# Performance work log

Hardware: AMD Instinct MI355X
Metric: run time of the kernel (lower is better)

## Reference

```python
import jax, jax.numpy as jnp
import numpy as np

D_MODEL = 1024
NHEAD = 16
HEAD_DIM = D_MODEL // NHEAD  # 64
THETA = 10000.0


def apply_rope(t):
    # t: [B, H, S, D]. Interleaved-pair RoPE (lucidrains rotary-embedding-torch
    # rotate_queries_or_keys), positions = arange(S), theta = 10000.
    B, H, S, D = t.shape
    inv_freq = 1.0 / (THETA ** (jnp.arange(0, D, 2, dtype=jnp.float32) / D))  # [D/2]
    ang = jnp.arange(S, dtype=jnp.float32)[:, None] * inv_freq               # [S, D/2]
    cos = jnp.cos(ang).astype(t.dtype)
    sin = jnp.sin(ang).astype(t.dtype)
    tp = t.reshape(B, H, S, D // 2, 2)
    x1, x2 = tp[..., 0], tp[..., 1]
    rot = jnp.stack([x1 * cos - x2 * sin, x1 * sin + x2 * cos], axis=-1)
    return rot.reshape(B, H, S, D)


def setup_inputs() -> dict:
    key = jax.random.key(0)
    k0, k1, k2, k3, k4 = jax.random.split(key, 5)
    B, Sx, Sc = 2, 2048, 2048
    sc = 0.02  # weight init scale
    return {
        "x": jax.random.normal(k0, (B, Sx, D_MODEL), jnp.float32),
        "context": jax.random.normal(k1, (B, Sc, D_MODEL), jnp.float32),
        "Wq": jax.random.normal(k2, (D_MODEL, D_MODEL), jnp.float32) * sc,
        "Wv": jax.random.normal(k3, (D_MODEL, D_MODEL), jnp.float32) * sc,
        "Wo": jax.random.normal(k4, (D_MODEL, D_MODEL), jnp.float32) * sc,
        "bo": jnp.zeros((D_MODEL,), jnp.float32),
        "x_pos": jnp.arange(B * Sx, dtype=jnp.int64).reshape(B, Sx) % Sx,
        "context_pos": jnp.arange(B * Sc, dtype=jnp.int64).reshape(B, Sc) % Sc,
    }


def reference(x, context, Wq, Wv, Wo, bo, x_pos, context_pos):
    # x_pos/context_pos are unused when both streams use the internal
    # RotaryEmbedding (is_imu1=is_imu2=True), matching the original forward.
    B, Sx, _ = x.shape
    Sc = context.shape[1]
    q = (x @ Wq.T).reshape(B, Sx, NHEAD, HEAD_DIM).transpose(0, 2, 1, 3)
    # NOTE: original code uses projq (not projk) for keys — replicated here.
    k = (context @ Wq.T).reshape(B, Sc, NHEAD, HEAD_DIM).transpose(0, 2, 1, 3)
    v = (context @ Wv.T).reshape(B, Sc, NHEAD, HEAD_DIM).transpose(0, 2, 1, 3)
    q = apply_rope(q)
    k = apply_rope(k)
    scale = 1.0 / jnp.sqrt(jnp.asarray(HEAD_DIM, q.dtype))
    attn = jax.nn.softmax(jnp.einsum("bhqd,bhkd->bhqk", q, k) * scale, axis=-1)
    out = jnp.einsum("bhqk,bhkd->bhqd", attn, v)            # [B,H,Sx,hd]
    out = out.transpose(0, 2, 1, 3).reshape(B, Sx, D_MODEL)  # [B,Sx,d_model]
    return out @ Wo.T + bo
```

## Files before the change

kernel.cpp:

```cpp
#include <hip/hip_runtime.h>
#include <cmath>


typedef __bf16 bf16x8 __attribute__((ext_vector_type(8)));
typedef __bf16 bf16x4 __attribute__((ext_vector_type(4)));
typedef float f32x4 __attribute__((ext_vector_type(4)));
typedef float f32x16 __attribute__((ext_vector_type(16)));
typedef unsigned u32x4v __attribute__((ext_vector_type(4)));

#define MFMA(A, B, C) __builtin_amdgcn_mfma_f32_16x16x32_bf16(A, B, C, 0, 0, 0)
#define MFMA32(A, B, C) __builtin_amdgcn_mfma_f32_32x32x16_bf16(A, B, C, 0, 0, 0)
#define GLL16(g, l)                                                        \
  __builtin_amdgcn_global_load_lds(                                        \
      (const __attribute__((address_space(1))) unsigned int*)(g),          \
      (__attribute__((address_space(3))) unsigned int*)(l), 16, 0, 0)

#define WAITB(N)                                          \
  do {                                                    \
    asm volatile("s_waitcnt vmcnt(" #N ")" ::: "memory"); \
    __builtin_amdgcn_s_barrier();                         \
  } while (0)

__global__ __launch_bounds__(256) void cvt_all_kernel(
    const float* __restrict__ x, const float* __restrict__ ctx,
    const float* __restrict__ Wq, const float* __restrict__ Wv,
    const float* __restrict__ Wo, __bf16* __restrict__ xb, __bf16* __restrict__ cb,
    __bf16* __restrict__ Wqb, __bf16* __restrict__ Wvb, __bf16* __restrict__ Wob) {
  int base = blockIdx.x * 512 + threadIdx.x;
  const float* src;
  __bf16* dst;
  int off;
  if (base < 1048576) { src = x; dst = xb; off = 0; }
  else if (base < 2097152) { src = ctx; dst = cb; off = 1048576; }
  else if (base < 2359296) { src = Wq; dst = Wqb; off = 2097152; }
  else if (base < 2621440) { src = Wv; dst = Wvb; off = 2359296; }
  else { src = Wo; dst = Wob; off = 2621440; }
#pragma unroll
  for (int jj = 0; jj < 2; jj++) {
    int j = base - off + jj * 256;
    float4 f = ((const float4*)src)[j];
    bf16x4 o;
    o[0] = (__bf16)f.x; o[1] = (__bf16)f.y; o[2] = (__bf16)f.z; o[3] = (__bf16)f.w;
    ((bf16x4*)dst)[j] = o;
  }
}

__global__ __launch_bounds__(256) void gemm_proj(const __bf16* __restrict__ A0,
                                                 const __bf16* __restrict__ W0,
                                                 void* __restrict__ outQ,
                                                 void* __restrict__ outK,
                                                 void* __restrict__ outV) {
  const int tid = threadIdx.x;
  const int wave = tid >> 6, lane = tid & 63, quad = lane >> 4, l15 = lane & 15;
  const int mw = wave >> 1, nw = wave & 1;

  const int id = blockIdx.x;
  int m0, n0;
  const __bf16* A;
  const __bf16* W;
  bool vmode;
  if (id < 512) {
    const int xcd = id & 7, j = id >> 3;
    m0 = (xcd * 8 + (j & 7)) * 128;
    n0 = (j >> 3) * 128;
    A = A0;
    W = W0;
    vmode = false;
  } else {
    const int vid = id - 512;
    const int xcd = vid & 7, j = vid >> 3;
    m0 = (xcd * 4 + (j & 3)) * 128;
    n0 = (j >> 2) * 128;
    A = A0 + (size_t)4096 * 1024;
    W = W0 + (size_t)1024 * 1024;
    vmode = true;
  }

  __shared__ __attribute__((aligned(16))) __bf16 As[3][4096];
  __shared__ __attribute__((aligned(16))) __bf16 Ws[3][4096];

  int goff[2];
#pragma unroll
  for (int jj = 0; jj < 2; jj++) {
    const int s = jj * 256 + tid;
    const int row = s >> 2;
    const int kcg = (s & 3) ^ ((row >> 1) & 3);
    goff[jj] = row * 1024 + kcg * 8;
  }
  const __bf16* Ag = A + (size_t)m0 * 1024;
  const __bf16* Wg = W + (size_t)n0 * 1024;
  const int ldsoff0 = wave * 512;
  const int ldsoff1 = 2048 + wave * 512;

  const int sw = (l15 >> 1) & 3;
  int afoff[4], wfoff[4];
#pragma unroll
  for (int t = 0; t < 4; t++) {
    afoff[t] = (mw * 64 + t * 16 + l15) * 32 + (quad ^ sw) * 8;
    wfoff[t] = (nw * 64 + t * 16 + l15) * 32 + (quad ^ sw) * 8;
  }

  f32x4 acc[4][4] = {};

  auto stage = [&](int buf, int k0) {
    GLL16(Ag + goff[0] + k0, &As[buf][ldsoff0]);
    GLL16(Ag + goff[1] + k0, &As[buf][ldsoff1]);
    GLL16(Wg + goff[0] + k0, &Ws[buf][ldsoff0]);
    GLL16(Wg + goff[1] + k0, &Ws[buf][ldsoff1]);
  };
  auto compute = [&](int buf) {
    bf16x8 af[4], wf[4];
#pragma unroll
    for (int t = 0; t < 4; t++) af[t] = *(const bf16x8*)&As[buf][afoff[t]];
#pragma unroll
    for (int t = 0; t < 4; t++) wf[t] = *(const bf16x8*)&Ws[buf][wfoff[t]];
#pragma unroll
    for (int mt = 0; mt < 4; mt++)
#pragma unroll
      for (int nt = 0; nt < 4; nt++) acc[mt][nt] = MFMA(af[mt], wf[nt], acc[mt][nt]);
  };

  stage(0, 0);
  stage(1, 32);
  int buf = 0;
  for (int c = 0; c < 31; c++) {
    WAITB(4);
    if (c + 2 < 32) {
      int nb = buf + 2;
      if (nb >= 3) nb -= 3;
      stage(nb, (c + 2) * 32);
    }
    compute(buf);
    buf = (buf == 2) ? 0 : buf + 1;
  }
  WAITB(0);
  compute(buf);

  if (!vmode) {
    const int isK = (m0 >= 4096);
    __bf16* O = (__bf16*)(isK ? outK : outQ);
    const float qsc = isK ? 1.0f : 0.18033688f;
    const int mb = m0 & 4095;
#pragma unroll
    for (int nt = 0; nt < 4; nt++) {
      const int n = n0 + nw * 64 + nt * 16 + l15;
      const int h = n >> 6, d = n & 63, p = d >> 1;
      const float invf_rev =
          __builtin_amdgcn_exp2f(-((float)p * 0.41524101f + 2.6514961f));
#pragma unroll
      for (int mt = 0; mt < 4; mt++) {
#pragma unroll
        for (int r = 0; r < 4; r++) {
          const int row = mb + mw * 64 + mt * 16 + quad * 4 + r;
          const int s = row & 2047, b = row >> 11;
          float v = acc[mt][nt][r];
          float pv = __shfl_xor(v, 1, 64);
          float fr = __builtin_amdgcn_fractf((float)s * invf_rev);
          float sn = __builtin_amdgcn_sinf(fr);
          float cs = __builtin_amdgcn_cosf(fr);
          float res = (lane & 1) ? (pv * sn + v * cs) : (v * cs - pv * sn);
          O[((size_t)(b * 16 + h) * 2048 + s) * 64 + d] = (__bf16)(res * qsc);
        }
      }
    }
  } else {
    __bf16* O = (__bf16*)outV;
#pragma unroll
    for (int nt = 0; nt < 4; nt++) {
      const int n = n0 + nw * 64 + nt * 16 + l15;
      const int h = n >> 6, d = n & 63;
#pragma unroll
      for (int mt = 0; mt < 4; mt++) {
        const int rowb = m0 + mw * 64 + mt * 16 + quad * 4;
        const int s = rowb & 2047, b = rowb >> 11;
        bf16x4 o;
#pragma unroll
        for (int r = 0; r < 4; r++) o[r] = (__bf16)acc[mt][nt][r];
        *(bf16x4*)(O + ((size_t)(b * 16 + h) * 64 + d) * 2048 + s) = o;
      }
    }
  }
}

__global__ __launch_bounds__(256) void gemm_out(const __bf16* __restrict__ A,
                                                const __bf16* __restrict__ W,
                                                float* __restrict__ O,
                                                const float* __restrict__ bias) {
  const int tid = threadIdx.x;
  const int wave = tid >> 6, lane = tid & 63, quad = lane >> 4, l15 = lane & 15;
  const int mw = wave >> 1, nw = wave & 1;
  const int id = blockIdx.x;
  const int xcd = id & 7, j = id >> 3;
  const int m0 = (xcd * 4 + (j & 3)) * 128;
  const int n0 = (j >> 2) * 64;

  __shared__ __attribute__((aligned(16))) __bf16 As[3][4096];
  __shared__ __attribute__((aligned(16))) __bf16 Ws[3][2048];

  int goff[2];
#pragma unroll
  for (int jj = 0; jj < 2; jj++) {
    const int s = jj * 256 + tid;
    const int row = s >> 2;
    const int kcg = (s & 3) ^ ((row >> 1) & 3);
    goff[jj] = row * 1024 + kcg * 8;
  }
  const int wrow = tid >> 2;
  const int wkcg = (tid & 3) ^ ((wrow >> 1) & 3);
  const int goffw = wrow * 1024 + wkcg * 8;

  const __bf16* Ag = A + (size_t)m0 * 1024;
  const __bf16* Wg = W + (size_t)n0 * 1024;
  const int ldsoff0 = wave * 512;
  const int ldsoff1 = 2048 + wave * 512;

  const int sw = (l15 >> 1) & 3;
  int afoff[4], wfoff[2];
#pragma unroll
  for (int t = 0; t < 4; t++)
    afoff[t] = (mw * 64 + t * 16 + l15) * 32 + (quad ^ sw) * 8;
#pragma unroll
  for (int t = 0; t < 2; t++)
    wfoff[t] = (nw * 32 + t * 16 + l15) * 32 + (quad ^ sw) * 8;

  f32x4 acc[4][2] = {};

  auto stage = [&](int buf, int k0) {
    GLL16(Ag + goff[0] + k0, &As[buf][ldsoff0]);
    GLL16(Ag + goff[1] + k0, &As[buf][ldsoff1]);
    GLL16(Wg + goffw + k0, &Ws[buf][ldsoff0]);
  };
  auto compute = [&](int buf) {
    bf16x8 af[4], wf[2];
#pragma unroll
    for (int t = 0; t < 4; t++) af[t] = *(const bf16x8*)&As[buf][afoff[t]];
#pragma unroll
    for (int t = 0; t < 2; t++) wf[t] = *(const bf16x8*)&Ws[buf][wfoff[t]];
#pragma unroll
    for (int mt = 0; mt < 4; mt++)
#pragma unroll
      for (int nt = 0; nt < 2; nt++) acc[mt][nt] = MFMA(af[mt], wf[nt], acc[mt][nt]);
  };

  stage(0, 0);
  stage(1, 32);
  int buf = 0;
  for (int c = 0; c < 31; c++) {
    WAITB(3);
    if (c + 2 < 32) {
      int nb = buf + 2;
      if (nb >= 3) nb -= 3;
      stage(nb, (c + 2) * 32);
    }
    compute(buf);
    buf = (buf == 2) ? 0 : buf + 1;
  }
  WAITB(0);
  compute(buf);

#pragma unroll
  for (int nt = 0; nt < 2; nt++) {
    const int n = n0 + nw * 32 + nt * 16 + l15;
    const float bv = bias[n];
#pragma unroll
    for (int mt = 0; mt < 4; mt++) {
#pragma unroll
      for (int r = 0; r < 4; r++) {
        const int row = m0 + mw * 64 + mt * 16 + quad * 4 + r;
        O[(size_t)row * 1024 + n] = acc[mt][nt][r] + bv;
      }
    }
  }
}

__global__ __launch_bounds__(512, 4) void attn_kernel(const __bf16* __restrict__ Q,
                                                      const __bf16* __restrict__ K,
                                                      const __bf16* __restrict__ Vt,
                                                      __bf16* __restrict__ Aout) {
  const int tid = threadIdx.x;
  const int wave = tid >> 6, lane = tid & 63;
  const int l31 = lane & 31, hi = lane >> 5;
  const int qg = wave >> 1, kg = wave & 1;
  const int id = blockIdx.x;
  const int j = id >> 3;
  const int bh = ((id & 7) << 2) | (j & 3);
  const int q0 = (j >> 2) << 7;

  const __bf16* Qb = Q + (size_t)bh * (2048 * 64);
  const __bf16* Kb = K + (size_t)bh * (2048 * 64);
  const __bf16* Vb = Vt + (size_t)bh * (64 * 2048);

  __shared__ __attribute__((aligned(16))) __bf16 Kbuf[4][4096];
  __shared__ __attribute__((aligned(16))) __bf16 Vbuf[4][4096];

  bf16x8 qf[4];
  {
    const __bf16* qp = Qb + (size_t)(q0 + qg * 32 + l31) * 64 + hi * 8;
#pragma unroll
    for (int i = 0; i < 4; i++) qf[i] = *(const bf16x8*)(qp + i * 16);
  }

  const int s0 = wave * 64 + lane;
  const int r0 = s0 >> 3, c0 = (s0 & 7) ^ (r0 & 7);
  const __bf16* kgp = Kb + r0 * 64 + c0 * 8;
  const __bf16* vgp = Vb + r0 * 2048 + c0 * 8;
  const int klds = wave * 512;

  int koff[4];
  {
    const int rk = kg * 32 + l31;
#pragma unroll
    for (int i = 0; i < 4; i++) koff[i] = rk * 64 + (((2 * i + hi) ^ (rk & 7)) * 8);
  }
  int voff[2][2];
#pragma unroll
  for (int dt = 0; dt < 2; dt++) {
    const int rv = dt * 32 + l31;
#pragma unroll
    for (int ks = 0; ks < 2; ks++)
      voff[dt][ks] = rv * 64 + (((kg * 4 + ks * 2 + hi) ^ (rv & 7)) * 8);
  }

  f32x4 rs4 = {};
  f32x16 oacc[2] = {};

  auto stage = [&](int buf, int kt) {
    GLL16(kgp + kt * 64, &Kbuf[buf][klds]);
    GLL16(vgp + kt, &Vbuf[buf][klds]);
  };

  auto compute = [&](int buf) {
    f32x16 s = {};
#pragma unroll
    for (int i = 0; i < 4; i++) {
      bf16x8 kf = *(const bf16x8*)&Kbuf[buf][koff[i]];
      s = MFMA32(kf, qf[i], s);
    }
    float pe[16];
#pragma unroll
    for (int r = 0; r < 16; r++) pe[r] = __builtin_amdgcn_exp2f(s[r]);
#pragma unroll
    for (int r = 0; r < 16; r++) rs4[r & 3] += pe[r];
    bf16x8 pa[2];
#pragma unroll
    for (int sl = 0; sl < 2; sl++) {
      unsigned wa, wb, wc, wd;
      asm("v_cvt_pk_bf16_f32 %0, %1, %2" : "=v"(wa) : "v"(pe[8 * sl + 0]), "v"(pe[8 * sl + 1]));
      asm("v_cvt_pk_bf16_f32 %0, %1, %2" : "=v"(wb) : "v"(pe[8 * sl + 4]), "v"(pe[8 * sl + 5]));
      asm("v_cvt_pk_bf16_f32 %0, %1, %2" : "=v"(wc) : "v"(pe[8 * sl + 2]), "v"(pe[8 * sl + 3]));
      asm("v_cvt_pk_bf16_f32 %0, %1, %2" : "=v"(wd) : "v"(pe[8 * sl + 6]), "v"(pe[8 * sl + 7]));
      asm("v_permlane32_swap_b32 %0, %1" : "+v"(wa), "+v"(wb));
      asm("v_permlane32_swap_b32 %0, %1" : "+v"(wc), "+v"(wd));
      u32x4v t;
      t[0] = wa; t[1] = wc; t[2] = wb; t[3] = wd;
      pa[sl] = __builtin_bit_cast(bf16x8, t);
    }
#pragma unroll
    for (int dt = 0; dt < 2; dt++)
#pragma unroll
      for (int ks = 0; ks < 2; ks++) {
        bf16x8 vf = *(const bf16x8*)&Vbuf[buf][voff[dt][ks]];
        oacc[dt] = MFMA32(pa[ks], vf, oacc[dt]);
      }
  };

  stage(0, 0);
  stage(1, 64);
  for (int kt = 0; kt < 2048; kt += 128) {
    const int p = (kt >> 7) & 1;
    __syncthreads();
    if (kt + 128 < 2048) {
      stage(2 * (p ^ 1), kt + 128);
      stage(2 * (p ^ 1) + 1, kt + 192);
    }
    compute(2 * p);
    compute(2 * p + 1);
  }

  __syncthreads();
  float* Ored = (float*)&Kbuf[0][0];
  float* Lred = (float*)&Vbuf[0][0];

  float lw = (rs4[0] + rs4[1]) + (rs4[2] + rs4[3]);
  lw += __shfl_xor(lw, 32, 64);
  Lred[wave * 64 + lane] = lw;
  if (kg == 1) {
#pragma unroll
    for (int dt = 0; dt < 2; dt++)
#pragma unroll
      for (int r = 0; r < 16; r++)
        Ored[(qg * 32 + dt * 16 + r) * 64 + lane] = oacc[dt][r];
  }
  __syncthreads();
  if (kg == 0) {
    const int b = bh >> 4, h = bh & 15;
#pragma unroll
    for (int r = 0; r < 16; r++) {
      const int qrow = (r & 3) + 8 * (r >> 2) + 4 * hi;
      const float lt =
          Lred[(qg * 2) * 64 + qrow] + Lred[(qg * 2 + 1) * 64 + qrow];
      const float inv = 1.f / lt;
      const int qAbs = q0 + qg * 32 + qrow;
#pragma unroll
      for (int dt = 0; dt < 2; dt++) {
        const float o = oacc[dt][r] + Ored[(qg * 32 + dt * 16 + r) * 64 + lane];
        Aout[((size_t)(b * 2048 + qAbs)) * 1024 + h * 64 + dt * 32 + l31] =
            (__bf16)(o * inv);
      }
    }
  }
}

extern "C" void kernel_launch(void* const* d_in, const int* in_sizes, int n_in,
                              void* d_out, int out_size, void* d_ws, size_t ws_size,
                              hipStream_t stream) {
  const float* x   = (const float*)d_in[0];
  const float* ctx = (const float*)d_in[1];
  const float* Wq  = (const float*)d_in[2];
  const float* Wv  = (const float*)d_in[3];
  const float* Wo  = (const float*)d_in[4];
  const float* bo  = (const float*)d_in[5];

  char* ws = (char*)d_ws;
  const size_t MB = 1024 * 1024;
  __bf16* xb   = (__bf16*)(ws + 0 * MB);
  __bf16* cb   = (__bf16*)(ws + 8 * MB);
  __bf16* Wqb  = (__bf16*)(ws + 16 * MB);
  __bf16* Wvb  = (__bf16*)(ws + 18 * MB);
  __bf16* Wob  = (__bf16*)(ws + 20 * MB);
  __bf16* qh   = (__bf16*)(ws + 22 * MB);
  __bf16* kh   = (__bf16*)(ws + 30 * MB);
  __bf16* vt   = (__bf16*)(ws + 38 * MB);
  __bf16* attn = xb;

  cvt_all_kernel<<<5632, 256, 0, stream>>>(x, ctx, Wq, Wv, Wo, xb, cb, Wqb, Wvb, Wob);

  gemm_proj<<<768, 256, 0, stream>>>(xb, Wqb, (void*)qh, (void*)kh, (void*)vt);

  attn_kernel<<<512, 512, 0, stream>>>(qh, kh, vt, attn);

  gemm_out<<<512, 256, 0, stream>>>(attn, Wob, (float*)d_out, bo);
}
```

Measured before the change: 210.7 us.

## Retile projection GEMM to 256x256 blocks with a 4-stage pipeline

The Q/K/V projection GEMM moves from 128x128 tiles with 256 threads to 256x256 tiles with 512 threads (8 waves), which raises operand reuse per LDS load. It uses a 4-slot global-to-LDS pipeline with three tiles in flight, and raises wave priority around the MFMA bursts with s_setprio. Only 192 blocks are launched, fewer than the number of CUs, and the larger LDS footprint limits residency, so load balance and latency hiding may suffer. The output GEMM's loop now uses a full __syncthreads in place of the partial vmcnt wait, which drains all loads at every step and reduces overlap there.

```diff
diff --git a/kernel.cpp b/kernel.cpp
--- a/kernel.cpp
+++ b/kernel.cpp
@@ -45,96 +45,100 @@
   }
 }
 
-__global__ __launch_bounds__(256) void gemm_proj(const __bf16* __restrict__ A0,
-                                                 const __bf16* __restrict__ W0,
-                                                 void* __restrict__ outQ,
-                                                 void* __restrict__ outK,
-                                                 void* __restrict__ outV) {
+__global__ __launch_bounds__(512, 2) void gemm_proj(const __bf16* __restrict__ A0,
+                                                    const __bf16* __restrict__ W0,
+                                                    void* __restrict__ outQ,
+                                                    void* __restrict__ outK,
+                                                    void* __restrict__ outV) {
   const int tid = threadIdx.x;
   const int wave = tid >> 6, lane = tid & 63, quad = lane >> 4, l15 = lane & 15;
-  const int mw = wave >> 1, nw = wave & 1;
+  const int wm = wave >> 2, wn = wave & 3;
 
   const int id = blockIdx.x;
   int m0, n0;
   const __bf16* A;
   const __bf16* W;
   bool vmode;
-  if (id < 512) {
+  if (id < 128) {
     const int xcd = id & 7, j = id >> 3;
-    m0 = (xcd * 8 + (j & 7)) * 128;
-    n0 = (j >> 3) * 128;
+    m0 = (xcd * 4 + (j & 3)) * 256;
+    n0 = (j >> 2) * 256;
     A = A0;
     W = W0;
     vmode = false;
   } else {
-    const int vid = id - 512;
+    const int vid = id - 128;
     const int xcd = vid & 7, j = vid >> 3;
-    m0 = (xcd * 4 + (j & 3)) * 128;
-    n0 = (j >> 2) * 128;
+    m0 = (xcd * 2 + (j & 1)) * 256;
+    n0 = (j >> 1) * 256;
     A = A0 + (size_t)4096 * 1024;
     W = W0 + (size_t)1024 * 1024;
     vmode = true;
   }
 
-  __shared__ __attribute__((aligned(16))) __bf16 As[3][4096];
-  __shared__ __attribute__((aligned(16))) __bf16 Ws[3][4096];
-
-  int goff[2];
-#pragma unroll
-  for (int jj = 0; jj < 2; jj++) {
-    const int s = jj * 256 + tid;
-    const int row = s >> 2;
-    const int kcg = (s & 3) ^ ((row >> 1) & 3);
-    goff[jj] = row * 1024 + kcg * 8;
-  }
+  __shared__ __attribute__((aligned(16))) __bf16 As[4][8192];
+  __shared__ __attribute__((aligned(16))) __bf16 Ws[4][8192];
+
+  const int srow = tid >> 2;
+  const int kcg = (tid & 3) ^ ((srow >> 1) & 3);
+  const int aoff = srow * 1024 + kcg * 8;
   const __bf16* Ag = A + (size_t)m0 * 1024;
   const __bf16* Wg = W + (size_t)n0 * 1024;
-  const int ldsoff0 = wave * 512;
-  const int ldsoff1 = 2048 + wave * 512;
+  const int ldst = wave * 512;
 
   const int sw = (l15 >> 1) & 3;
-  int afoff[4], wfoff[4];
-#pragma unroll
-  for (int t = 0; t < 4; t++) {
-    afoff[t] = (mw * 64 + t * 16 + l15) * 32 + (quad ^ sw) * 8;
-    wfoff[t] = (nw * 64 + t * 16 + l15) * 32 + (quad ^ sw) * 8;
-  }
-
-  f32x4 acc[4][4] = {};
-
-  auto stage = [&](int buf, int k0) {
-    GLL16(Ag + goff[0] + k0, &As[buf][ldsoff0]);
-    GLL16(Ag + goff[1] + k0, &As[buf][ldsoff1]);
-    GLL16(Wg + goff[0] + k0, &Ws[buf][ldsoff0]);
-    GLL16(Wg + goff[1] + k0, &Ws[buf][ldsoff1]);
-  };
-  auto compute = [&](int buf) {
-    bf16x8 af[4], wf[4];
-#pragma unroll
-    for (int t = 0; t < 4; t++) af[t] = *(const bf16x8*)&As[buf][afoff[t]];
-#pragma unroll
-    for (int t = 0; t < 4; t++) wf[t] = *(const bf16x8*)&Ws[buf][wfoff[t]];
-#pragma unroll
-    for (int mt = 0; mt < 4; mt++)
-#pragma unroll
-      for (int nt = 0; nt < 4; nt++) acc[mt][nt] = MFMA(af[mt], wf[nt], acc[mt][nt]);
-  };
-
-  stage(0, 0);
-  stage(1, 32);
-  int buf = 0;
-  for (int c = 0; c < 31; c++) {
-    WAITB(4);
-    if (c + 2 < 32) {
-      int nb = buf + 2;
-      if (nb >= 3) nb -= 3;
-      stage(nb, (c + 2) * 32);
-    }
-    compute(buf);
-    buf = (buf == 2) ? 0 : buf + 1;
-  }
+  const int xoff = (quad ^ sw) * 8;
+
+  f32x4 acc[8][4] = {};
+
+  auto stage = [&](int t) {
+    const int slot = t & 3;
+    const int ko = t * 32;
+    GLL16(Ag + aoff + ko,          &As[slot][ldst]);
+    GLL16(Ag + aoff + 131072 + ko, &As[slot][4096 + ldst]);
+    GLL16(Wg + aoff + ko,          &Ws[slot][ldst]);
+    GLL16(Wg + aoff + 131072 + ko, &Ws[slot][4096 + ldst]);
+  };
+
+  auto compute = [&](int slot) {
+    bf16x8 bf[4], af[4];
+#pragma unroll
+    for (int nf = 0; nf < 4; nf++)
+      bf[nf] = *(const bf16x8*)&Ws[slot][(wn * 64 + nf * 16 + l15) * 32 + xoff];
+#pragma unroll
+    for (int mf = 0; mf < 4; mf++)
+      af[mf] = *(const bf16x8*)&As[slot][(wm * 128 + mf * 16 + l15) * 32 + xoff];
+    __builtin_amdgcn_s_setprio(1);
+#pragma unroll
+    for (int mf = 0; mf < 4; mf++)
+#pragma unroll
+      for (int nf = 0; nf < 4; nf++)
+        acc[mf][nf] = MFMA(af[mf], bf[nf], acc[mf][nf]);
+    __builtin_amdgcn_s_setprio(0);
+#pragma unroll
+    for (int mf = 0; mf < 4; mf++)
+      af[mf] = *(const bf16x8*)&As[slot][(wm * 128 + (4 + mf) * 16 + l15) * 32 + xoff];
+    __builtin_amdgcn_s_setprio(1);
+#pragma unroll
+    for (int mf = 0; mf < 4; mf++)
+#pragma unroll
+      for (int nf = 0; nf < 4; nf++)
+        acc[4 + mf][nf] = MFMA(af[mf], bf[nf], acc[4 + mf][nf]);
+    __builtin_amdgcn_s_setprio(0);
+  };
+
+  stage(0);
+  stage(1);
+  stage(2);
+  for (int t = 0; t < 30; t++) {
+    WAITB(8);
+    if (t < 29) stage(t + 3);
+    compute(t & 3);
+  }
+  WAITB(4);
+  compute(2);
   WAITB(0);
-  compute(buf);
+  compute(3);
 
   if (!vmode) {
     const int isK = (m0 >= 4096);
@@ -142,18 +146,18 @@
     const float qsc = isK ? 1.0f : 0.18033688f;
     const int mb = m0 & 4095;
 #pragma unroll
-    for (int nt = 0; nt < 4; nt++) {
-      const int n = n0 + nw * 64 + nt * 16 + l15;
+    for (int nf = 0; nf < 4; nf++) {
+      const int n = n0 + wn * 64 + nf * 16 + l15;
       const int h = n >> 6, d = n & 63, p = d >> 1;
       const float invf_rev =
           __builtin_amdgcn_exp2f(-((float)p * 0.41524101f + 2.6514961f));
 #pragma unroll
-      for (int mt = 0; mt < 4; mt++) {
+      for (int mf = 0; mf < 8; mf++) {
 #pragma unroll
         for (int r = 0; r < 4; r++) {
-          const int row = mb + mw * 64 + mt * 16 + quad * 4 + r;
+          const int row = mb + wm * 128 + mf * 16 + quad * 4 + r;
           const int s = row & 2047, b = row >> 11;
-          float v = acc[mt][nt][r];
+          float v = acc[mf][nf][r];
           float pv = __shfl_xor(v, 1, 64);
           float fr = __builtin_amdgcn_fractf((float)s * invf_rev);
           float sn = __builtin_amdgcn_sinf(fr);
@@ -166,16 +170,16 @@
   } else {
     __bf16* O = (__bf16*)outV;
 #pragma unroll
-    for (int nt = 0; nt < 4; nt++) {
-      const int n = n0 + nw * 64 + nt * 16 + l15;
+    for (int nf = 0; nf < 4; nf++) {
+      const int n = n0 + wn * 64 + nf * 16 + l15;
       const int h = n >> 6, d = n & 63;
 #pragma unroll
-      for (int mt = 0; mt < 4; mt++) {
-        const int rowb = m0 + mw * 64 + mt * 16 + quad * 4;
+      for (int mf = 0; mf < 8; mf++) {
+        const int rowb = m0 + wm * 128 + mf * 16 + quad * 4;
         const int s = rowb & 2047, b = rowb >> 11;
         bf16x4 o;
 #pragma unroll
-        for (int r = 0; r < 4; r++) o[r] = (__bf16)acc[mt][nt][r];
+        for (int r = 0; r < 4; r++) o[r] = (__bf16)acc[mf][nf][r];
         *(bf16x4*)(O + ((size_t)(b * 16 + h) * 64 + d) * 2048 + s) = o;
       }
     }
@@ -245,8 +249,8 @@
   stage(0, 0);
   stage(1, 32);
   int buf = 0;
-  for (int c = 0; c < 31; c++) {
-    WAITB(3);
+  for (int c = 0; c < 32; c++) {
+    __syncthreads();
     if (c + 2 < 32) {
       int nb = buf + 2;
       if (nb >= 3) nb -= 3;
@@ -255,8 +259,6 @@
     compute(buf);
     buf = (buf == 2) ? 0 : buf + 1;
   }
-  WAITB(0);
-  compute(buf);
 
 #pragma unroll
   for (int nt = 0; nt < 2; nt++) {
@@ -435,7 +437,7 @@
 
   cvt_all_kernel<<<5632, 256, 0, stream>>>(x, ctx, Wq, Wv, Wo, xb, cb, Wqb, Wvb, Wob);
 
-  gemm_proj<<<768, 256, 0, stream>>>(xb, Wqb, (void*)qh, (void*)kh, (void*)vt);
+  gemm_proj<<<192, 512, 0, stream>>>(xb, Wqb, (void*)qh, (void*)kh, (void*)vt);
 
   attn_kernel<<<512, 512, 0, stream>>>(qh, kh, vt, attn);
 
```

Result: faster. 203.1 us (-3.6%).
